# Performance work log

Hardware: AMD Instinct MI355X
Metric: run time of the kernel (lower is better)

The kernel has to match this reference:

```python
import jax, jax.numpy as jnp
import numpy as np

N, E, DI, DO = 50000, 800000, 64, 64
EPS = 1e-06


def setup_inputs() -> dict:
    key = jax.random.key(0)
    ks = jax.random.split(key, 8)
    # xavier_uniform bounds: sqrt(6/(fan_in+fan_out))
    bf_f = float(np.sqrt(6.0 / (2 * DI + DO)))
    bf_w = float(np.sqrt(6.0 / (2 * DI + 1)))
    return {
        "x": jax.random.normal(ks[0], (N, DI), dtype=jnp.float32),
        "adj": jnp.zeros((1,), dtype=jnp.float32),  # unused in forward
        "src": jax.random.randint(ks[1], (E,), 0, N),
        "tgt": jax.random.randint(ks[2], (E,), 0, N),
        "Msrc": jnp.zeros((1,), dtype=jnp.float32),  # unused in forward
        "Wf": jax.random.uniform(ks[3], (DO, 2 * DI), jnp.float32, -bf_f, bf_f),
        "bf": jnp.zeros((DO,), dtype=jnp.float32),
        "Ww": jax.random.uniform(ks[4], (1, 2 * DI), jnp.float32, -bf_w, bf_w),
        "bw": jnp.zeros((1,), dtype=jnp.float32),
    }


def reference(x, adj, src, tgt, Msrc, Wf, bf, Ww, bw):
    n_nodes = x.shape[0]
    # edge gather + concat: h is [E, 2*di]
    h = jnp.concatenate([x[src], x[tgt]], axis=1)
    y = jax.nn.relu(h @ Wf.T + bf)          # [E, do]
    a = h @ Ww.T + bw                        # [E, 1]
    # Mtgt @ v  ==  segment_sum(v, tgt) since Mtgt is the target one-hot matrix
    a_sum = jax.ops.segment_sum(a, tgt, num_segments=n_nodes) + EPS   # [N, 1]
    o = jax.ops.segment_sum(y * a, tgt, num_segments=n_nodes) / a_sum  # [N, do]
    return o
```

## Files before the change

kernel.cpp:

```cpp
#include <hip/hip_runtime.h>
#include <hip/hip_bf16.h>


#define NBLK 200

__global__ __launch_bounds__(256) void gat_pre_hist(
    const float* __restrict__ x, const float* __restrict__ Wf,
    const float* __restrict__ Ww, const float* __restrict__ bf,
    const float* __restrict__ bw,
    __hip_bfloat16* __restrict__ A16, float* __restrict__ B,
    float* __restrict__ cg, float* __restrict__ dg, int N,
    const int* __restrict__ tgt, int* __restrict__ counts,
    int E, int NB, int chunk, int nb1)
{
    __shared__ float w2[64][132];
    __shared__ float xs[64][68];
    __shared__ float ww[128];
    __shared__ float bfs[64];
    __shared__ int   h[256];

    const int tid = threadIdx.x;

    if (blockIdx.x >= nb1) {
        const int k = blockIdx.x - nb1;
        h[tid] = 0;
        __syncthreads();
        const int lo = k * chunk;
        const int hi = min(lo + chunk, E);
        for (int e = lo + tid; e < hi; e += 256)
            atomicAdd(&h[tgt[e] >> 8], 1);
        __syncthreads();
        if (tid < NB) counts[tid * NBLK + k] = h[tid];
        return;
    }

    for (int f = tid; f < 64 * 128; f += 256) {
        int d  = f >> 7;
        int kk = f & 127;
        w2[kk & 63][(kk >> 6) * 64 + d] = Wf[f];
    }
    if (tid < 128) ww[tid] = Ww[tid];
    if (tid < 64)  bfs[tid] = bf[tid];

    const int n0 = blockIdx.x << 6;
    for (int i = tid; i < 64 * 64; i += 256) {
        int nl = i >> 6, k = i & 63;
        int n = n0 + nl;
        xs[k][nl] = (n < N) ? x[(size_t)n * 64 + k] : 0.f;
    }
    __syncthreads();

    const int ti = tid & 15, tj = tid >> 4;
    float acc[4][8];
#pragma unroll
    for (int i = 0; i < 4; ++i)
#pragma unroll
        for (int j = 0; j < 8; ++j) acc[i][j] = 0.f;

#pragma unroll 4
    for (int k = 0; k < 64; ++k) {
        const float4 xv = *(const float4*)&xs[k][ti * 4];
        const float4 w0 = *(const float4*)&w2[k][tj * 8];
        const float4 w1 = *(const float4*)&w2[k][tj * 8 + 4];
        const float xa[4] = {xv.x, xv.y, xv.z, xv.w};
        const float wa[8] = {w0.x, w0.y, w0.z, w0.w, w1.x, w1.y, w1.z, w1.w};
#pragma unroll
        for (int i = 0; i < 4; ++i)
#pragma unroll
            for (int j = 0; j < 8; ++j)
                acc[i][j] = fmaf(xa[i], wa[j], acc[i][j]);
    }

#pragma unroll
    for (int i = 0; i < 4; ++i) {
        const int n = n0 + ti * 4 + i;
        if (n < N) {
            if (tj < 8) {
#pragma unroll
                for (int j = 0; j < 8; ++j)
                    A16[(size_t)n * 64 + tj * 8 + j] = __float2bfloat16(acc[i][j]);
            } else {
#pragma unroll
                for (int j = 0; j < 8; ++j) {
                    int d2 = (tj - 8) * 8 + j;
                    B[(size_t)n * 64 + d2] = acc[i][j] + bfs[d2];
                }
            }
        }
    }

    if (tid < 64) {
        const int n = n0 + tid;
        if (n < N) {
            float sc = 0.f, sd = 0.f;
            for (int k = 0; k < 64; ++k) {
                const float xv = xs[k][tid];
                sc = fmaf(xv, ww[k], sc);
                sd = fmaf(xv, ww[64 + k], sd);
            }
            cg[n] = sc;
            dg[n] = sd + bw[0];
        }
    }
}

__global__ __launch_bounds__(256) void gat_scan1(
    const int* __restrict__ in, int* __restrict__ out,
    int* __restrict__ bsum, int n)
{
    __shared__ int tmp[256];
    const int i = blockIdx.x * 256 + threadIdx.x;
    const int v = (i < n) ? in[i] : 0;
    tmp[threadIdx.x] = v;
    __syncthreads();
#pragma unroll
    for (int off = 1; off < 256; off <<= 1) {
        const int add = (threadIdx.x >= off) ? tmp[threadIdx.x - off] : 0;
        __syncthreads();
        tmp[threadIdx.x] += add;
        __syncthreads();
    }
    if (i < n) out[i] = tmp[threadIdx.x] - v;
    if (threadIdx.x == 255) bsum[blockIdx.x] = tmp[255];
}

__global__ __launch_bounds__(1024) void gat_scan2(int* __restrict__ bsum, int nb)
{
    __shared__ int tmp[1024];
    const int v = (threadIdx.x < nb) ? bsum[threadIdx.x] : 0;
    tmp[threadIdx.x] = v;
    __syncthreads();
#pragma unroll
    for (int off = 1; off < 1024; off <<= 1) {
        const int add = (threadIdx.x >= off) ? tmp[threadIdx.x - off] : 0;
        __syncthreads();
        tmp[threadIdx.x] += add;
        __syncthreads();
    }
    if (threadIdx.x < nb) bsum[threadIdx.x] = tmp[threadIdx.x] - v;
}

__global__ __launch_bounds__(256) void gat_scan3(
    int* __restrict__ data, const int* __restrict__ bsum, int n)
{
    const int i = blockIdx.x * 256 + threadIdx.x;
    if (i < n) data[i] += bsum[blockIdx.x];
}

__global__ __launch_bounds__(256) void gat_partition(
    const int* __restrict__ src, const int* __restrict__ tgt,
    const int* __restrict__ psum, int2* __restrict__ pairs,
    int E, int NB, int chunk)
{
    __shared__ int cur[256];
    const int k = blockIdx.x;
    const int tid = threadIdx.x;
    if (tid < NB) cur[tid] = psum[tid * NBLK + k];
    __syncthreads();
    const int lo = k * chunk;
    const int hi = min(lo + chunk, E);
    for (int e = lo + tid; e < hi; e += 256) {
        const int t = tgt[e];
        const int s = src[e];
        const int pos = atomicAdd(&cur[t >> 8], 1);
        pairs[pos] = make_int2(s, t);
    }
}

__global__ __launch_bounds__(256) void gat_bucket_sort(
    const int2* __restrict__ pairs, const int* __restrict__ psum,
    int* __restrict__ starts, int* __restrict__ sorted_src,
    int N, int E, int NB)
{
    __shared__ int h[256];
    __shared__ int cur[256];
    const int b = blockIdx.x;
    const int tid = threadIdx.x;
    const int base = psum[b * NBLK];
    const int end  = (b + 1 < NB) ? psum[(b + 1) * NBLK] : E;

    h[tid] = 0;
    __syncthreads();
    for (int e = base + tid; e < end; e += 256)
        atomicAdd(&h[pairs[e].y & 255], 1);
    __syncthreads();
    const int v = h[tid];
#pragma unroll
    for (int off = 1; off < 256; off <<= 1) {
        const int add = (tid >= off) ? h[tid - off] : 0;
        __syncthreads();
        h[tid] += add;
        __syncthreads();
    }
    const int excl = h[tid] - v;
    const int node = (b << 8) + tid;
    if (node < N) starts[node] = base + excl;
    if (b == NB - 1 && tid == 0) starts[N] = E;
    cur[tid] = base + excl;
    __syncthreads();
    for (int e = base + tid; e < end; e += 256) {
        const int2 p = pairs[e];
        const int pos = atomicAdd(&cur[p.y & 255], 1);
        sorted_src[pos] = p.x;
    }
}

__global__ __launch_bounds__(256) void gat_gather(
    const int* __restrict__ starts, const int* __restrict__ sorted_src,
    const __hip_bfloat16* __restrict__ A16, const float* __restrict__ B,
    const float* __restrict__ cg, const float* __restrict__ dg,
    float* __restrict__ out, int N)
{
    const int d = threadIdx.x & 63;
    const int node = blockIdx.x * (blockDim.x >> 6) + (threadIdx.x >> 6);
    if (node >= N) return;
    const int e0 = starts[node];
    const int e1 = starts[node + 1];
    const float Bt  = B[(size_t)node * 64 + d];
    const float dgt = dg[node];
    float acc = 0.f, asum = 0.f;

    int e = e0;
    for (; e + 3 < e1; e += 4) {
        const int s0 = sorted_src[e];
        const int s1 = sorted_src[e + 1];
        const int s2 = sorted_src[e + 2];
        const int s3 = sorted_src[e + 3];
        const float a0 = cg[s0] + dgt;
        const float a1 = cg[s1] + dgt;
        const float a2 = cg[s2] + dgt;
        const float a3 = cg[s3] + dgt;
        const float x0 = __bfloat162float(A16[(size_t)s0 * 64 + d]);
        const float x1 = __bfloat162float(A16[(size_t)s1 * 64 + d]);
        const float x2 = __bfloat162float(A16[(size_t)s2 * 64 + d]);
        const float x3 = __bfloat162float(A16[(size_t)s3 * 64 + d]);
        acc = fmaf(fmaxf(x0 + Bt, 0.f), a0, acc);
        acc = fmaf(fmaxf(x1 + Bt, 0.f), a1, acc);
        acc = fmaf(fmaxf(x2 + Bt, 0.f), a2, acc);
        acc = fmaf(fmaxf(x3 + Bt, 0.f), a3, acc);
        asum += (a0 + a1) + (a2 + a3);
    }
    for (; e < e1; ++e) {
        const int s   = sorted_src[e];
        const float a = cg[s] + dgt;
        const float xv = __bfloat162float(A16[(size_t)s * 64 + d]);
        acc = fmaf(fmaxf(xv + Bt, 0.f), a, acc);
        asum += a;
    }
    out[(size_t)node * 64 + d] = acc / (asum + 1e-6f);
}

extern "C" void kernel_launch(void* const* d_in, const int* in_sizes, int n_in,
                              void* d_out, int out_size, void* d_ws, size_t ws_size,
                              hipStream_t stream)
{
    const float* x   = (const float*)d_in[0];
    const int*   src = (const int*)d_in[2];
    const int*   tgt = (const int*)d_in[3];
    const float* Wf  = (const float*)d_in[5];
    const float* bf  = (const float*)d_in[6];
    const float* Ww  = (const float*)d_in[7];
    const float* bw  = (const float*)d_in[8];

    const int N = in_sizes[0] / 64;
    const int E = in_sizes[2];
    float* out = (float*)d_out;

    const int NB    = (N + 255) >> 8;
    const int chunk = (E + NBLK - 1) / NBLK;
    const int NBNB  = NB * NBLK;

    int2* pairs = (int2*)d_out;

    __hip_bfloat16* A16 = (__hip_bfloat16*)d_ws;
    float* B          = (float*)(A16 + (size_t)N * 64);
    float* cg         = B + (size_t)N * 64;
    float* dg         = cg + N;
    int*   starts     = (int*)(dg + N);
    int*   sorted_src = starts + N + 1;
    int*   counts     = sorted_src + E;
    int*   bsum       = counts + NBNB;

    const int nb1 = (N + 63) / 64;
    gat_pre_hist<<<nb1 + NBLK, 256, 0, stream>>>(x, Wf, Ww, bf, bw, A16, B, cg, dg, N,
                                                 tgt, counts, E, NB, chunk, nb1);
    const int nbs = (NBNB + 255) / 256;
    gat_scan1<<<nbs, 256, 0, stream>>>(counts, counts, bsum, NBNB);
    gat_scan2<<<1, 1024, 0, stream>>>(bsum, nbs);
    gat_scan3<<<nbs, 256, 0, stream>>>(counts, bsum, NBNB);
    gat_partition<<<NBLK, 256, 0, stream>>>(src, tgt, counts, pairs, E, NB, chunk);
    gat_bucket_sort<<<NB, 256, 0, stream>>>(pairs, counts, starts, sorted_src, N, E, NB);
    const int nb2 = (N + 3) / 4;
    gat_gather<<<nb2, 256, 0, stream>>>(starts, sorted_src, A16, B, cg, dg, out, N);
}
```

Measured before the change: 95.68 us.

## Fold scan fixup into consumers, pack edge pairs, unroll gather by eight

Removes the scan3 launch by having the partition and bucket-sort kernels add the block offset from bsum when they read the prefix counts. Packs each (src, tgt-low-byte) pair into one 32-bit word instead of an int2, halving the traffic of the partition scratch buffer. This assumes src fits in 24 bits. Adds an 8-way unrolled loop in the gather kernel to keep more independent loads in flight per node.

```diff
diff --git a/kernel.cpp b/kernel.cpp
--- a/kernel.cpp
+++ b/kernel.cpp
@@ -140,22 +140,18 @@
     if (threadIdx.x < nb) bsum[threadIdx.x] = tmp[threadIdx.x] - v;
 }
 
-__global__ __launch_bounds__(256) void gat_scan3(
-    int* __restrict__ data, const int* __restrict__ bsum, int n)
-{
-    const int i = blockIdx.x * 256 + threadIdx.x;
-    if (i < n) data[i] += bsum[blockIdx.x];
-}
-
 __global__ __launch_bounds__(256) void gat_partition(
     const int* __restrict__ src, const int* __restrict__ tgt,
-    const int* __restrict__ psum, int2* __restrict__ pairs,
-    int E, int NB, int chunk)
+    const int* __restrict__ counts, const int* __restrict__ bsum,
+    unsigned int* __restrict__ pairs, int E, int NB, int chunk)
 {
     __shared__ int cur[256];
     const int k = blockIdx.x;
     const int tid = threadIdx.x;
-    if (tid < NB) cur[tid] = psum[tid * NBLK + k];
+    if (tid < NB) {
+        const int idx = tid * NBLK + k;
+        cur[tid] = counts[idx] + bsum[idx >> 8];
+    }
     __syncthreads();
     const int lo = k * chunk;
     const int hi = min(lo + chunk, E);
@@ -163,12 +159,13 @@
         const int t = tgt[e];
         const int s = src[e];
         const int pos = atomicAdd(&cur[t >> 8], 1);
-        pairs[pos] = make_int2(s, t);
+        pairs[pos] = ((unsigned int)s << 8) | (unsigned int)(t & 255);
     }
 }
 
 __global__ __launch_bounds__(256) void gat_bucket_sort(
-    const int2* __restrict__ pairs, const int* __restrict__ psum,
+    const unsigned int* __restrict__ pairs, const int* __restrict__ counts,
+    const int* __restrict__ bsum,
     int* __restrict__ starts, int* __restrict__ sorted_src,
     int N, int E, int NB)
 {
@@ -176,13 +173,18 @@
     __shared__ int cur[256];
     const int b = blockIdx.x;
     const int tid = threadIdx.x;
-    const int base = psum[b * NBLK];
-    const int end  = (b + 1 < NB) ? psum[(b + 1) * NBLK] : E;
+    const int i0 = b * NBLK;
+    const int base = counts[i0] + bsum[i0 >> 8];
+    int end = E;
+    if (b + 1 < NB) {
+        const int i1 = (b + 1) * NBLK;
+        end = counts[i1] + bsum[i1 >> 8];
+    }
 
     h[tid] = 0;
     __syncthreads();
     for (int e = base + tid; e < end; e += 256)
-        atomicAdd(&h[pairs[e].y & 255], 1);
+        atomicAdd(&h[pairs[e] & 255u], 1);
     __syncthreads();
     const int v = h[tid];
 #pragma unroll
@@ -199,9 +201,9 @@
     cur[tid] = base + excl;
     __syncthreads();
     for (int e = base + tid; e < end; e += 256) {
-        const int2 p = pairs[e];
-        const int pos = atomicAdd(&cur[p.y & 255], 1);
-        sorted_src[pos] = p.x;
+        const unsigned int p = pairs[e];
+        const int pos = atomicAdd(&cur[p & 255u], 1);
+        sorted_src[pos] = (int)(p >> 8);
     }
 }
 
@@ -221,6 +223,22 @@
     float acc = 0.f, asum = 0.f;
 
     int e = e0;
+    for (; e + 7 < e1; e += 8) {
+        int s[8];
+#pragma unroll
+        for (int u = 0; u < 8; ++u) s[u] = sorted_src[e + u];
+        float a[8], xv[8];
+#pragma unroll
+        for (int u = 0; u < 8; ++u) a[u] = cg[s[u]] + dgt;
+#pragma unroll
+        for (int u = 0; u < 8; ++u)
+            xv[u] = __bfloat162float(A16[(size_t)s[u] * 64 + d]);
+#pragma unroll
+        for (int u = 0; u < 8; ++u) {
+            acc = fmaf(fmaxf(xv[u] + Bt, 0.f), a[u], acc);
+            asum += a[u];
+        }
+    }
     for (; e + 3 < e1; e += 4) {
         const int s0 = sorted_src[e];
         const int s1 = sorted_src[e + 1];
@@ -270,7 +288,7 @@
     const int chunk = (E + NBLK - 1) / NBLK;
     const int NBNB  = NB * NBLK;
 
-    int2* pairs = (int2*)d_out;
+    unsigned int* pairs = (unsigned int*)d_out;
 
     __hip_bfloat16* A16 = (__hip_bfloat16*)d_ws;
     float* B          = (float*)(A16 + (size_t)N * 64);
@@ -287,9 +305,8 @@
     const int nbs = (NBNB + 255) / 256;
     gat_scan1<<<nbs, 256, 0, stream>>>(counts, counts, bsum, NBNB);
     gat_scan2<<<1, 1024, 0, stream>>>(bsum, nbs);
-    gat_scan3<<<nbs, 256, 0, stream>>>(counts, bsum, NBNB);
-    gat_partition<<<NBLK, 256, 0, stream>>>(src, tgt, counts, pairs, E, NB, chunk);
-    gat_bucket_sort<<<NB, 256, 0, stream>>>(pairs, counts, starts, sorted_src, N, E, NB);
+    gat_partition<<<NBLK, 256, 0, stream>>>(src, tgt, counts, bsum, pairs, E, NB, chunk);
+    gat_bucket_sort<<<NB, 256, 0, stream>>>(pairs, counts, bsum, starts, sorted_src, N, E, NB);
     const int nb2 = (N + 3) / 4;
     gat_gather<<<nb2, 256, 0, stream>>>(starts, sorted_src, A16, B, cg, dg, out, N);
 }
```

After: 88.46 us. -7.5%, faster.
